# Kernel tuning notes

Measured on AMD Instinct MI355X. Metric: run time of the kernel, lower is better.

Reference implementation:

```python
import jax, jax.numpy as jnp
import numpy as np

B, N, H, D, N_HEADS = 8, 2048, 1024, 1, 8
SCALE = H / N_HEADS  # 128.0 ; note: NOT sqrt, faithful to source


def _linear(x, w, b):
    # torch nn.Linear: y = x @ W^T + b ; w: [out, in]
    return jnp.einsum('bnh,oh->bno', x, w) + b


def setup_inputs() -> dict:
    key = jax.random.key(0)
    ks = jax.random.split(key, 18)
    s = 0.02
    inp = {
        'node_t': jax.random.normal(ks[0], (B, N, H), dtype=jnp.float32),
        'node_next': jax.random.normal(ks[1], (B, N, H), dtype=jnp.float32),
        'WQ_w': s * jax.random.normal(ks[2], (H, H), dtype=jnp.float32),
        'WQ_b': s * jax.random.normal(ks[3], (H,), dtype=jnp.float32),
        'WK_w': s * jax.random.normal(ks[4], (H, H), dtype=jnp.float32),
        'WK_b': s * jax.random.normal(ks[5], (H,), dtype=jnp.float32),
        'WV_w': s * jax.random.normal(ks[6], (H, H), dtype=jnp.float32),
        'WV_b': s * jax.random.normal(ks[7], (H,), dtype=jnp.float32),
        'WO_w': s * jax.random.normal(ks[8], (H, H), dtype=jnp.float32),
        'WO_b': s * jax.random.normal(ks[9], (H,), dtype=jnp.float32),
        'WE_w': s * jax.random.normal(ks[10], (H, H), dtype=jnp.float32),
        'WE_b': s * jax.random.normal(ks[11], (H,), dtype=jnp.float32),
        'WN_w': s * jax.random.normal(ks[12], (H, H), dtype=jnp.float32),
        'WN_b': s * jax.random.normal(ks[13], (H,), dtype=jnp.float32),
        'WA_w': s * jax.random.normal(ks[14], (D, H), dtype=jnp.float32),
        'WA_b': s * jax.random.normal(ks[15], (D,), dtype=jnp.float32),
    }
    return inp


def reference(node_t, node_next, WQ_w, WQ_b, WK_w, WK_b, WV_w, WV_b,
              WO_w, WO_b, WE_w, WE_b, WN_w, WN_b, WA_w, WA_b):
    Q = _linear(node_t, WQ_w, WQ_b)       # [B,N,H]
    K = _linear(node_next, WK_w, WK_b)    # [B,N,H]
    V = _linear(node_next, WV_w, WV_b)    # [B,N,H]
    att = jnp.einsum('bih,bkh->bik', Q, K)  # [B,N,N]
    # torch nn.Softmax() with no dim on a 3-D tensor -> legacy dim=0 (batch axis)
    att = jax.nn.softmax(att / SCALE, axis=0)
    # einsum('bnn,bnd->bnd') uses only the diagonal att[b,n,n]
    diag = jnp.einsum('bnn->bn', att)  # [B,N]
    av = diag[:, :, None] * V          # [B,N,H]
    h = jax.nn.gelu(_linear(av, WO_w, WO_b), approximate=False)  # exact erf GELU
    A_t = _linear(node_t, WE_w, WE_b) + _linear(h, WN_w, WN_b)   # [B,N,H]
    A_t = _linear(A_t, WA_w, WA_b)     # [B,N,1]
    return jnp.squeeze(A_t, axis=-1)   # [B,N]
```

## Files before the change

kernel.cpp:

```cpp
#include <hip/hip_runtime.h>
#include <cstdint>
#include <cstddef>


typedef __attribute__((ext_vector_type(8))) short bfx8;
typedef __attribute__((ext_vector_type(4))) short s16x4;
typedef __attribute__((ext_vector_type(4))) float f32x4;

#define N_SEQ 2048
#define M_TOT 16384
#define NT 16

__device__ __forceinline__ unsigned short f2bf(float f) {
  unsigned int u = __float_as_uint(f);
  return (unsigned short)((u + 0x7fffu + ((u >> 16) & 1u)) >> 16);
}
__device__ __forceinline__ float bf2f(short s) {
  return __uint_as_float(((unsigned int)(unsigned short)s) << 16);
}
__device__ __forceinline__ float gelu_exact(float g) {
  return 0.5f * g * (1.0f + erff(g * 0.70710678118654752f));
}
__device__ __forceinline__ void gload16(const void* g, void* l) {
  __builtin_amdgcn_global_load_lds(
      (const __attribute__((address_space(1))) unsigned int*)g,
      (__attribute__((address_space(3))) unsigned int*)(unsigned int)(uintptr_t)l,
      16, 0, 0);
}
__device__ __forceinline__ float dot4(float4 a, float4 b) {
  return a.x * b.x + a.y * b.y + a.z * b.z + a.w * b.w;
}

__global__ __launch_bounds__(256) void prep_w(
    const float* __restrict__ WQ, const float* __restrict__ WK,
    const float* __restrict__ WV, const float* __restrict__ WO,
    const float* __restrict__ WE, const float* __restrict__ WN,
    const float* __restrict__ wa, const float* __restrict__ bQ,
    const float* __restrict__ bK, const float* __restrict__ bV,
    const float* __restrict__ WEb, const float* __restrict__ WNb,
    const float* __restrict__ WAb,
    short* __restrict__ wqT, short* __restrict__ wkT,
    short* __restrict__ wvT, short* __restrict__ wo_bf,
    float* __restrict__ vE, float* __restrict__ vN,
    float* __restrict__ uQ, float* __restrict__ uK,
    float* __restrict__ c0, float* __restrict__ c1,
    float* __restrict__ bvw) {
  __shared__ short tile[64][65];
  __shared__ float redw[4];
  int bid = blockIdx.x, t = threadIdx.x;
  if (bid < 1024) {
    int z = bid >> 8, idx = bid & 255, bi = idx >> 4, bj = idx & 15;
    const float* src = z == 0 ? WQ : z == 1 ? WK : z == 2 ? WV : WO;
    if (z == 3) {
#pragma unroll
      for (int i = 0; i < 16; ++i) {
        int lin = i * 256 + t, r = lin >> 6, c = lin & 63;
        size_t idx2 = (size_t)(bi * 64 + r) * 1024 + bj * 64 + c;
        wo_bf[idx2] = (short)f2bf(src[idx2]);
      }
      return;
    }
    short* dst = z == 0 ? wqT : z == 1 ? wkT : wvT;
#pragma unroll
    for (int i = 0; i < 16; ++i) {
      int lin = i * 256 + t, r = lin >> 6, c = lin & 63;
      tile[r][c] = (short)f2bf(src[(size_t)(bi * 64 + r) * 1024 + bj * 64 + c]);
    }
    __syncthreads();
#pragma unroll
    for (int i = 0; i < 16; ++i) {
      int lin = i * 256 + t, r = lin >> 6, c = lin & 63;
      dst[(size_t)(bj * 64 + r) * 1024 + bi * 64 + c] = tile[c][r];
    }
  } else if (bid < 1280) {
    int idx = bid - 1024;
    int y = idx >> 6, ob = idx & 63;
    const float* M = y == 0 ? WE : y == 1 ? WN : y == 2 ? WQ : WK;
    const float* wv = (y < 2) ? wa : (y == 2 ? bK : bQ);
    float* dst = y == 0 ? vE : y == 1 ? vN : y == 2 ? uQ : uK;
    float a0 = 0.f, a1 = 0.f, a2 = 0.f, a3 = 0.f;
    int o0 = ob * 16;
#pragma unroll
    for (int i = 0; i < 16; ++i) {
      int o = o0 + i;
      float wvv = wv[o];
      const float* row = M + (size_t)o * 1024;
      a0 += wvv * row[t];
      a1 += wvv * row[t + 256];
      a2 += wvv * row[t + 512];
      a3 += wvv * row[t + 768];
    }
    atomicAdd(dst + t, a0);
    atomicAdd(dst + t + 256, a1);
    atomicAdd(dst + t + 512, a2);
    atomicAdd(dst + t + 768, a3);
  } else if (bid < 1282) {
    int which = bid - 1280;
    float a = 0.f;
    if (which == 0)
      for (int i = t; i < 1024; i += 256) a += wa[i] * (WEb[i] + WNb[i]);
    else
      for (int i = t; i < 1024; i += 256) a += bQ[i] * bK[i];
#pragma unroll
    for (int o = 32; o > 0; o >>= 1) a += __shfl_down(a, o, 64);
    if ((t & 63) == 0) redw[t >> 6] = a;
    __syncthreads();
    if (t == 0) {
      float tot = redw[0] + redw[1] + redw[2] + redw[3];
      if (which == 0) c0[0] = tot + WAb[0];
      else c1[0] = tot;
    }
  } else {
    int r = bid - 1282;
    float4 wv = ((const float4*)(WO + (size_t)r * 1024))[t];
    float4 bv = ((const float4*)bV)[t];
    float a = dot4(wv, bv);
#pragma unroll
    for (int o = 32; o > 0; o >>= 1) a += __shfl_down(a, o, 64);
    if ((t & 63) == 0) redw[t >> 6] = a;
    __syncthreads();
    if (t == 0) bvw[r] = redw[0] + redw[1] + redw[2] + redw[3];
  }
}

__global__ __launch_bounds__(256) void prep2(
    const short* __restrict__ wqT, const short* __restrict__ wkT,
    const short* __restrict__ wvT, const short* __restrict__ wo_bf,
    short* __restrict__ M1, short* __restrict__ M2,
    const float* __restrict__ nn, const float* __restrict__ nt,
    const float* __restrict__ uK, const float* __restrict__ vE,
    short* __restrict__ xn, float* __restrict__ xk,
    float* __restrict__ xe) {
  __shared__ short sA[128 * 64];
  __shared__ short sB[128 * 64];
  int bid = blockIdx.x, tid = threadIdx.x;
  if (bid >= 128) {
    int lane = tid & 63, wv = tid >> 6;
    int isNT = bid >= 2176;
    int idx = bid - (isNT ? 2176 : 128);
    const float* srcm = isNT ? nt : nn;
    const float* vec = isNT ? vE : uK;
    const float4* v4 = (const float4*)vec + lane * 4;
    float4 u0 = v4[0], u1 = v4[1], u2 = v4[2], u3 = v4[3];
    int row = idx * 8 + wv * 2;
#pragma unroll
    for (int rr = 0; rr < 2; ++rr) {
      const float4* src = (const float4*)(srcm + (size_t)(row + rr) * 1024)
                          + lane * 4;
      float4 a0 = src[0], a1 = src[1], a2 = src[2], a3 = src[3];
      if (!isNT) {
        bfx8 o0, o1;
        o0[0] = (short)f2bf(a0.x); o0[1] = (short)f2bf(a0.y);
        o0[2] = (short)f2bf(a0.z); o0[3] = (short)f2bf(a0.w);
        o0[4] = (short)f2bf(a1.x); o0[5] = (short)f2bf(a1.y);
        o0[6] = (short)f2bf(a1.z); o0[7] = (short)f2bf(a1.w);
        o1[0] = (short)f2bf(a2.x); o1[1] = (short)f2bf(a2.y);
        o1[2] = (short)f2bf(a2.z); o1[3] = (short)f2bf(a2.w);
        o1[4] = (short)f2bf(a3.x); o1[5] = (short)f2bf(a3.y);
        o1[6] = (short)f2bf(a3.z); o1[7] = (short)f2bf(a3.w);
        bfx8* dst = (bfx8*)(xn + (size_t)(row + rr) * 1024 + lane * 16);
        dst[0] = o0; dst[1] = o1;
      }
      float a = dot4(a0, u0) + dot4(a1, u1) + dot4(a2, u2) + dot4(a3, u3);
#pragma unroll
      for (int o = 32; o > 0; o >>= 1) a += __shfl_xor(a, o, 64);
      if (lane == 0) (isNT ? xe : xk)[row + rr] = a;
    }
    return;
  }
  int z = bid >> 6, by = (bid >> 3) & 7, bx = bid & 7;
  const short* A = z ? wo_bf : wqT;
  const short* B = z ? wvT : wkT;
  short* D = z ? M2 : M1;
  int lane = tid & 63, w = tid >> 6;
  int wm = w >> 1, wn = w & 1;
  f32x4 acc[4][4] = {};
  int lrow = lane & 15, lk = (lane >> 4) * 8;
  int srow = lane >> 3, scol = (lane & 7) * 8;
  const short* Ag = A + (size_t)by * 128 * 1024;
  const short* Bg = B + (size_t)bx * 128 * 1024;
  for (int k0 = 0; k0 < 1024; k0 += 64) {
#pragma unroll
    for (int i = 0; i < 4; ++i) {
      int c = w * 4 + i;
      gload16(Ag + (size_t)(c * 8 + srow) * 1024 + k0 + scol, sA + c * 512);
      gload16(Bg + (size_t)(c * 8 + srow) * 1024 + k0 + scol, sB + c * 512);
    }
    __syncthreads();
#pragma unroll
    for (int kk = 0; kk < 64; kk += 32) {
      bfx8 af[4], bfr[4];
#pragma unroll
      for (int mi = 0; mi < 4; ++mi)
        af[mi] = *(const bfx8*)(sA + (wm * 64 + mi * 16 + lrow) * 64 + kk + lk);
#pragma unroll
      for (int nj = 0; nj < 4; ++nj)
        bfr[nj] = *(const bfx8*)(sB + (wn * 64 + nj * 16 + lrow) * 64 + kk + lk);
#pragma unroll
      for (int mi = 0; mi < 4; ++mi)
#pragma unroll
        for (int nj = 0; nj < 4; ++nj)
          acc[mi][nj] = __builtin_amdgcn_mfma_f32_16x16x32_bf16(
              af[mi], bfr[nj], acc[mi][nj], 0, 0, 0);
    }
    __syncthreads();
  }
  int r0 = by * 128 + wm * 64, cb2 = bx * 128 + wn * 64;
#pragma unroll
  for (int mi = 0; mi < 4; ++mi)
#pragma unroll
    for (int nj = 0; nj < 4; ++nj) {
      int col = cb2 + nj * 16 + lrow;
#pragma unroll
      for (int r = 0; r < 4; ++r) {
        int row = r0 + mi * 16 + (lane >> 4) * 4 + r;
        D[(size_t)row * 1024 + col] = (short)f2bf(acc[mi][nj][r]);
      }
    }
}

__global__ __launch_bounds__(512, 2) void gemm_main(
    const short* __restrict__ A, const short* __restrict__ Bf,
    const float* __restrict__ bias2, const float* __restrict__ nodet,
    float* __restrict__ sPart, short* __restrict__ vw) {
  __shared__ short sA[2][16384];
  __shared__ short sB[2][16384];
  int tid = threadIdx.x;
  int lane = tid & 63, w = tid >> 6;
  int wm = w >> 2, wn = w & 3;
  int wg = blockIdx.x;
  int work = (wg & 7) * 64 + (wg >> 3);
  int by = work >> 3, bx = work & 7;
  int lrow = lane & 15, g = lane >> 4;
  int sw0 = g ^ (lrow & 7);
  int sg = (lane & 7) ^ (lane >> 3);
  const short* Agt = A + ((size_t)(by * 256 + w * 32 + (lane >> 3))) * 1024 + sg * 8;
  const short* Bgt = Bf + ((size_t)(bx * 256 + w * 32 + (lane >> 3))) * 1024 + sg * 8;

  f32x4 acc[8][4] = {};

  auto stage = [&](int buf, int kt) {
    const short* ag = Agt + kt * 64;
    const short* bg = Bgt + kt * 64;
    short* la = &sA[buf][w * 2048];
    short* lb = &sB[buf][w * 2048];
#pragma unroll
    for (int i = 0; i < 4; ++i) {
      gload16(ag + i * 8192, la + i * 512);
      gload16(bg + i * 8192, lb + i * 512);
    }
  };

  stage(0, 0);
  int cur = 0;
  for (int kt = 0; kt < NT; ++kt) {
    if (kt + 1 < NT) {
      stage(cur ^ 1, kt + 1);
      asm volatile("s_waitcnt vmcnt(8)" ::: "memory");
    } else {
      asm volatile("s_waitcnt vmcnt(0)" ::: "memory");
    }
    __builtin_amdgcn_sched_barrier(0);
    __builtin_amdgcn_s_barrier();
    __builtin_amdgcn_sched_barrier(0);

    const short* sa = &sA[cur][0];
    const short* sb = &sB[cur][0];
    int brow = wn * 64 + lrow;
    int arow = wm * 128 + lrow;
    bfx8 bq[4][2];
#pragma unroll
    for (int nj = 0; nj < 4; ++nj) {
      bq[nj][0] = *(const bfx8*)(sb + (brow + nj * 16) * 64 + sw0 * 8);
      bq[nj][1] = *(const bfx8*)(sb + (brow + nj * 16) * 64 + (sw0 ^ 4) * 8);
    }
#pragma unroll
    for (int q = 0; q < 4; ++q) {
      bfx8 a00 = *(const bfx8*)(sa + (arow + (2 * q) * 16) * 64 + sw0 * 8);
      bfx8 a01 = *(const bfx8*)(sa + (arow + (2 * q) * 16) * 64 + (sw0 ^ 4) * 8);
      bfx8 a10 = *(const bfx8*)(sa + (arow + (2 * q + 1) * 16) * 64 + sw0 * 8);
      bfx8 a11 = *(const bfx8*)(sa + (arow + (2 * q + 1) * 16) * 64 + (sw0 ^ 4) * 8);
      __builtin_amdgcn_s_setprio(1);
#pragma unroll
      for (int nj = 0; nj < 4; ++nj) {
        acc[2 * q][nj] = __builtin_amdgcn_mfma_f32_16x16x32_bf16(
            a00, bq[nj][0], acc[2 * q][nj], 0, 0, 0);
        acc[2 * q][nj] = __builtin_amdgcn_mfma_f32_16x16x32_bf16(
            a01, bq[nj][1], acc[2 * q][nj], 0, 0, 0);
        acc[2 * q + 1][nj] = __builtin_amdgcn_mfma_f32_16x16x32_bf16(
            a10, bq[nj][0], acc[2 * q + 1][nj], 0, 0, 0);
        acc[2 * q + 1][nj] = __builtin_amdgcn_mfma_f32_16x16x32_bf16(
            a11, bq[nj][1], acc[2 * q + 1][nj], 0, 0, 0);
      }
      __builtin_amdgcn_s_setprio(0);
    }
    __builtin_amdgcn_sched_barrier(0);
    __builtin_amdgcn_s_barrier();
    __builtin_amdgcn_sched_barrier(0);
    cur ^= 1;
  }

  int row0 = by * 256 + wm * 128;
  int cb = bx * 256 + wn * 64;
  if (bx < 4) {
    float bias_nj[4];
#pragma unroll
    for (int nj = 0; nj < 4; ++nj) bias_nj[nj] = bias2[cb + nj * 16 + lrow];
    int px = bx * 4 + wn;
#pragma unroll
    for (int mi = 0; mi < 8; ++mi) {
#pragma unroll
      for (int r = 0; r < 4; ++r) {
        int row = row0 + mi * 16 + g * 4 + r;
        const float* xr = nodet + (size_t)row * 1024;
        float v = 0.f;
#pragma unroll
        for (int nj = 0; nj < 4; ++nj)
          v += (acc[mi][nj][r] + bias_nj[nj]) * xr[cb + nj * 16 + lrow];
        v += __shfl_xor(v, 1, 64);
        v += __shfl_xor(v, 2, 64);
        v += __shfl_xor(v, 4, 64);
        v += __shfl_xor(v, 8, 64);
        if (lrow == 0) sPart[(size_t)row * 16 + px] = v;
      }
    }
  } else {
#pragma unroll
    for (int mi = 0; mi < 8; ++mi)
#pragma unroll
      for (int nj = 0; nj < 4; ++nj) {
        int colv = cb - 1024 + nj * 16 + lrow;
        float bv = bias2[1024 + colv];
#pragma unroll
        for (int r = 0; r < 4; ++r) {
          int row = row0 + mi * 16 + g * 4 + r;
          vw[(size_t)row * 1024 + colv] = (short)f2bf(acc[mi][nj][r] + bv);
        }
      }
  }
}

__global__ __launch_bounds__(512) void out2_kernel(
    const short* __restrict__ vw, const float* __restrict__ sPart,
    const float* __restrict__ xe, const float* __restrict__ xk,
    const float* __restrict__ vN, const float* __restrict__ bO,
    const float* __restrict__ c0p, const float* __restrict__ c1p,
    float* __restrict__ out) {
  int n = blockIdx.x, t = threadIdx.x;
  __shared__ float sS[8];
  if (t < 128) {
    int b = t >> 4, j = t & 15;
    size_t row = (size_t)b * N_SEQ + n;
    float p = sPart[row * 16 + j];
    p += __shfl_xor(p, 1, 64);
    p += __shfl_xor(p, 2, 64);
    p += __shfl_xor(p, 4, 64);
    p += __shfl_xor(p, 8, 64);
    if (j == 0) sS[b] = p + xk[row] + c1p[0];
  }
  __syncthreads();
  int b = t >> 6, lane = t & 63;
  float m = sS[0];
#pragma unroll
  for (int i = 1; i < 8; ++i) m = fmaxf(m, sS[i]);
  float sum = 0.f, eb = 0.f;
#pragma unroll
  for (int i = 0; i < 8; ++i) {
    float e = expf((sS[i] - m) * (1.0f / 128.0f));
    sum += e;
    if (i == b) eb = e;
  }
  float d = eb / sum;
  size_t row = (size_t)b * N_SEQ + n;
  const s16x4* vv = (const s16x4*)(vw + row * 1024 + lane * 16);
  const float4* bo4 = (const float4*)bO + lane * 4;
  const float4* vn4 = (const float4*)vN + lane * 4;
  float a = 0.f;
#pragma unroll
  for (int q = 0; q < 4; ++q) {
    s16x4 v = vv[q];
    float4 bo = bo4[q], vn = vn4[q];
    float gx;
    gx = fmaf(d, bf2f(v[0]), bo.x); a += gelu_exact(gx) * vn.x;
    gx = fmaf(d, bf2f(v[1]), bo.y); a += gelu_exact(gx) * vn.y;
    gx = fmaf(d, bf2f(v[2]), bo.z); a += gelu_exact(gx) * vn.z;
    gx = fmaf(d, bf2f(v[3]), bo.w); a += gelu_exact(gx) * vn.w;
  }
#pragma unroll
  for (int o = 32; o > 0; o >>= 1) a += __shfl_xor(a, o, 64);
  if (lane == 0) out[row] = xe[row] + c0p[0] + a;
}

extern "C" void kernel_launch(void* const* d_in, const int* in_sizes, int n_in,
                              void* d_out, int out_size, void* d_ws,
                              size_t ws_size, hipStream_t stream) {
  const float* nt  = (const float*)d_in[0];
  const float* nn  = (const float*)d_in[1];
  const float* WQ  = (const float*)d_in[2];
  const float* bQ  = (const float*)d_in[3];
  const float* WK  = (const float*)d_in[4];
  const float* bK  = (const float*)d_in[5];
  const float* WV  = (const float*)d_in[6];
  const float* bV  = (const float*)d_in[7];
  const float* WO  = (const float*)d_in[8];
  const float* bO  = (const float*)d_in[9];
  const float* WE  = (const float*)d_in[10];
  const float* WEb = (const float*)d_in[11];
  const float* WN  = (const float*)d_in[12];
  const float* WNb = (const float*)d_in[13];
  const float* wa  = (const float*)d_in[14];
  const float* WAb = (const float*)d_in[15];
  float* out = (float*)d_out;

  char* w = (char*)d_ws;
  size_t o = 0;
  const size_t BIG = (size_t)M_TOT * 1024 * 2;
  short* xn     = (short*)(w + o); o += BIG;
  short* vw     = (short*)(w + o); o += BIG;
  short* Bf     = (short*)(w + o); o += (size_t)2048 * 1024 * 2;
  short* wqT    = (short*)(w + o); o += 2097152;
  short* wkT    = (short*)(w + o); o += 2097152;
  short* wvT    = (short*)(w + o); o += 2097152;
  short* wo_bf  = (short*)(w + o); o += 2097152;
  float* sPart  = (float*)(w + o); o += (size_t)M_TOT * 16 * 4;
  float* bias2  = (float*)(w + o); o += 8192;
  float* vE     = (float*)(w + o); o += 4096;
  float* vN     = (float*)(w + o); o += 4096;
  float* uK     = (float*)(w + o); o += 4096;
  float* xk     = (float*)(w + o); o += 65536;
  float* xe     = (float*)(w + o); o += 65536;
  float* c0     = (float*)(w + o); o += 256;
  float* c1     = (float*)(w + o); o += 256;
  (void)ws_size; (void)in_sizes; (void)n_in; (void)out_size;

  hipMemsetAsync(bias2, 0, 8192 + 4096 * 3, stream);

  prep_w<<<2306, 256, 0, stream>>>(WQ, WK, WV, WO, WE, WN, wa, bQ, bK, bV,
                                   WEb, WNb, WAb, wqT, wkT, wvT, wo_bf,
                                   vE, vN, bias2, uK, c0, c1, bias2 + 1024);
  prep2<<<4224, 256, 0, stream>>>(wqT, wkT, wvT, wo_bf, Bf, Bf + 1048576,
                                  nn, nt, uK, vE, xn, xk, xe);
  gemm_main<<<512, 512, 0, stream>>>(xn, Bf, bias2, nt, sPart, vw);
  out2_kernel<<<N_SEQ, 512, 0, stream>>>(vw, sPart, xe, xk, vN, bO,
                                         c0, c1, out);
}
```

Before: 152.0 us.

## Split GEMM LDS staging into half-tiles interleaved with MFMA phases

Restructures the main GEMM's double-buffered LDS pipeline. A and B tiles are split into halves and their global-to-LDS loads are issued inside the four MFMA sub-phases. B is prefetched two k-steps ahead, reusing the current buffer slot after its data is consumed. The aim is to spread memory traffic across the compute loop and shorten the exposed wait at each k-step boundary, at the cost of a barrier per sub-phase and tighter buffer-hazard ordering.

```diff
diff --git a/kernel.cpp b/kernel.cpp
--- a/kernel.cpp
+++ b/kernel.cpp
@@ -223,8 +223,8 @@
     const short* __restrict__ A, const short* __restrict__ Bf,
     const float* __restrict__ bias2, const float* __restrict__ nodet,
     float* __restrict__ sPart, short* __restrict__ vw) {
-  __shared__ short sA[2][16384];
-  __shared__ short sB[2][16384];
+  __shared__ short sA[2][2][8192];
+  __shared__ short sB[2][2][8192];
   int tid = threadIdx.x;
   int lane = tid & 63, w = tid >> 6;
   int wm = w >> 2, wn = w & 3;
@@ -233,71 +233,82 @@
   int by = work >> 3, bx = work & 7;
   int lrow = lane & 15, g = lane >> 4;
   int sw0 = g ^ (lrow & 7);
-  int sg = (lane & 7) ^ (lane >> 3);
-  const short* Agt = A + ((size_t)(by * 256 + w * 32 + (lane >> 3))) * 1024 + sg * 8;
-  const short* Bgt = Bf + ((size_t)(bx * 256 + w * 32 + (lane >> 3))) * 1024 + sg * 8;
+  int strow = tid >> 3;
+  int sgc = (tid & 7) ^ (strow & 7);
+  const short* Abase = A + (size_t)(by * 256 + strow) * 1024 + sgc * 8;
+  const short* Bbase = Bf + (size_t)(bx * 256 + strow) * 1024 + sgc * 8;
+  int lbase = w * 512;
 
   f32x4 acc[8][4] = {};
 
-  auto stage = [&](int buf, int kt) {
-    const short* ag = Agt + kt * 64;
-    const short* bg = Bgt + kt * 64;
-    short* la = &sA[buf][w * 2048];
-    short* lb = &sB[buf][w * 2048];
-#pragma unroll
-    for (int i = 0; i < 4; ++i) {
-      gload16(ag + i * 8192, la + i * 512);
-      gload16(bg + i * 8192, lb + i * 512);
-    }
+  auto stageA = [&](int db, int h, int kt) {
+#pragma unroll
+    for (int i = 0; i < 2; ++i)
+      gload16(Abase + (size_t)(h * 128 + i * 64) * 1024 + kt * 64,
+              &sA[db][h][i * 4096 + lbase]);
   };
-
-  stage(0, 0);
-  int cur = 0;
+  auto stageB = [&](int db, int h, int kt) {
+#pragma unroll
+    for (int i = 0; i < 2; ++i)
+      gload16(Bbase + (size_t)(h * 128 + i * 64) * 1024 + kt * 64,
+              &sB[db][h][i * 4096 + lbase]);
+  };
+
+  stageA(0, 0, 0); stageA(0, 1, 0);
+  stageB(0, 0, 0); stageB(0, 1, 0);
+  stageB(1, 0, 1); stageB(1, 1, 1);
+  asm volatile("s_waitcnt vmcnt(4)" ::: "memory");
+  __builtin_amdgcn_sched_barrier(0);
+  __builtin_amdgcn_s_barrier();
+  __builtin_amdgcn_sched_barrier(0);
+
+  int bh = wn >> 1, brw = (wn & 1) * 64 + lrow;
   for (int kt = 0; kt < NT; ++kt) {
-    if (kt + 1 < NT) {
-      stage(cur ^ 1, kt + 1);
-      asm volatile("s_waitcnt vmcnt(8)" ::: "memory");
-    } else {
-      asm volatile("s_waitcnt vmcnt(0)" ::: "memory");
-    }
+    int db = kt & 1;
+    const short* sa = &sA[db][wm][0];
+    const short* sb = &sB[db][bh][0];
+    bfx8 bq[4][2];
+#pragma unroll
+    for (int p = 0; p < 4; ++p) {
+      if (p == 0) {
+#pragma unroll
+        for (int nj = 0; nj < 4; ++nj) {
+          bq[nj][0] = *(const bfx8*)(sb + (brw + nj * 16) * 64 + sw0 * 8);
+          bq[nj][1] = *(const bfx8*)(sb + (brw + nj * 16) * 64 + (sw0 ^ 4) * 8);
+        }
+      }
+      bfx8 a00 = *(const bfx8*)(sa + ((2 * p) * 16 + lrow) * 64 + sw0 * 8);
+      bfx8 a01 = *(const bfx8*)(sa + ((2 * p) * 16 + lrow) * 64 + (sw0 ^ 4) * 8);
+      bfx8 a10 = *(const bfx8*)(sa + ((2 * p + 1) * 16 + lrow) * 64 + sw0 * 8);
+      bfx8 a11 = *(const bfx8*)(sa + ((2 * p + 1) * 16 + lrow) * 64 + (sw0 ^ 4) * 8);
+      if (p == 0 && kt + 1 < NT) stageA(db ^ 1, 0, kt + 1);
+      if (p == 1 && kt + 1 < NT) stageA(db ^ 1, 1, kt + 1);
+      if (p == 2 && kt + 2 < NT) stageB(db, 0, kt + 2);
+      if (p == 3 && kt + 2 < NT) stageB(db, 1, kt + 2);
+      __builtin_amdgcn_sched_barrier(0);
+      __builtin_amdgcn_s_barrier();
+      asm volatile("s_waitcnt lgkmcnt(0)" ::: "memory");
+      __builtin_amdgcn_sched_barrier(0);
+      __builtin_amdgcn_s_setprio(1);
+#pragma unroll
+      for (int nj = 0; nj < 4; ++nj) {
+        acc[2 * p][nj] = __builtin_amdgcn_mfma_f32_16x16x32_bf16(
+            a00, bq[nj][0], acc[2 * p][nj], 0, 0, 0);
+        acc[2 * p][nj] = __builtin_amdgcn_mfma_f32_16x16x32_bf16(
+            a01, bq[nj][1], acc[2 * p][nj], 0, 0, 0);
+        acc[2 * p + 1][nj] = __builtin_amdgcn_mfma_f32_16x16x32_bf16(
+            a10, bq[nj][0], acc[2 * p + 1][nj], 0, 0, 0);
+        acc[2 * p + 1][nj] = __builtin_amdgcn_mfma_f32_16x16x32_bf16(
+            a11, bq[nj][1], acc[2 * p + 1][nj], 0, 0, 0);
+      }
+      __builtin_amdgcn_s_setprio(0);
+      __builtin_amdgcn_sched_barrier(0);
+    }
+    if (kt < NT - 2)       asm volatile("s_waitcnt vmcnt(4)" ::: "memory");
+    else if (kt == NT - 2) asm volatile("s_waitcnt vmcnt(0)" ::: "memory");
     __builtin_amdgcn_sched_barrier(0);
     __builtin_amdgcn_s_barrier();
     __builtin_amdgcn_sched_barrier(0);
-
-    const short* sa = &sA[cur][0];
-    const short* sb = &sB[cur][0];
-    int brow = wn * 64 + lrow;
-    int arow = wm * 128 + lrow;
-    bfx8 bq[4][2];
-#pragma unroll
-    for (int nj = 0; nj < 4; ++nj) {
-      bq[nj][0] = *(const bfx8*)(sb + (brow + nj * 16) * 64 + sw0 * 8);
-      bq[nj][1] = *(const bfx8*)(sb + (brow + nj * 16) * 64 + (sw0 ^ 4) * 8);
-    }
-#pragma unroll
-    for (int q = 0; q < 4; ++q) {
-      bfx8 a00 = *(const bfx8*)(sa + (arow + (2 * q) * 16) * 64 + sw0 * 8);
-      bfx8 a01 = *(const bfx8*)(sa + (arow + (2 * q) * 16) * 64 + (sw0 ^ 4) * 8);
-      bfx8 a10 = *(const bfx8*)(sa + (arow + (2 * q + 1) * 16) * 64 + sw0 * 8);
-      bfx8 a11 = *(const bfx8*)(sa + (arow + (2 * q + 1) * 16) * 64 + (sw0 ^ 4) * 8);
-      __builtin_amdgcn_s_setprio(1);
-#pragma unroll
-      for (int nj = 0; nj < 4; ++nj) {
-        acc[2 * q][nj] = __builtin_amdgcn_mfma_f32_16x16x32_bf16(
-            a00, bq[nj][0], acc[2 * q][nj], 0, 0, 0);
-        acc[2 * q][nj] = __builtin_amdgcn_mfma_f32_16x16x32_bf16(
-            a01, bq[nj][1], acc[2 * q][nj], 0, 0, 0);
-        acc[2 * q + 1][nj] = __builtin_amdgcn_mfma_f32_16x16x32_bf16(
-            a10, bq[nj][0], acc[2 * q + 1][nj], 0, 0, 0);
-        acc[2 * q + 1][nj] = __builtin_amdgcn_mfma_f32_16x16x32_bf16(
-            a11, bq[nj][1], acc[2 * q + 1][nj], 0, 0, 0);
-      }
-      __builtin_amdgcn_s_setprio(0);
-    }
-    __builtin_amdgcn_sched_barrier(0);
-    __builtin_amdgcn_s_barrier();
-    __builtin_amdgcn_sched_barrier(0);
-    cur ^= 1;
   }
 
   int row0 = by * 256 + wm * 128;
```

After: 147.9 us. 1.03x faster.
